# Kernel tuning notes

Measured on AMD Instinct MI355X. Metric: run time of the kernel, lower is better.

## Reference

```python
import jax, jax.numpy as jnp
import numpy as np

IO_DIM = 64
WIDTH = 16
HID = 128
N = 500000
BS = IO_DIM * WIDTH  # block size for u and w
OUT = 2 * BS + WIDTH  # hypernet output size


def setup_inputs() -> dict:
    key = jax.random.key(0)
    ks = jax.random.split(key, 8)
    s = 0.1  # small init so tanh stays in its active range
    return {
        "t": jax.random.uniform(ks[0], (1,), jnp.float32),
        "z": jax.random.normal(ks[1], (N, IO_DIM), jnp.float32),
        "W1": jax.random.normal(ks[2], (HID, 1), jnp.float32) * s,
        "b1": jnp.zeros((HID,), jnp.float32),
        "W2": jax.random.normal(ks[3], (HID, HID), jnp.float32) * s,
        "b2": jnp.zeros((HID,), jnp.float32),
        "W3": jax.random.normal(ks[4], (OUT, HID), jnp.float32) * s,
        "b3": jax.random.normal(ks[5], (OUT,), jnp.float32) * s,
    }


def reference(t, z, W1, b1, W2, b2, W3, b3):
    # Hypernetwork: scalar t -> (u, w, b) for each of WIDTH blocks.
    h = jnp.tanh(W1 @ t + b1)            # [HID]
    h = jnp.tanh(W2 @ h + b2)            # [HID]
    uwb = W3 @ h + b3                    # [2*BS + WIDTH]

    u = uwb[:BS].reshape(WIDTH, IO_DIM)        # u_k row vectors
    w = uwb[BS:2 * BS].reshape(WIDTH, IO_DIM)  # w_k column vectors
    bb = uwb[2 * BS:]                          # [WIDTH] biases

    # dz/dt = mean_k tanh(z . w_k + b_k) u_k
    a = z @ w.T + bb                     # [N, WIDTH]
    th = jnp.tanh(a)                     # [N, WIDTH]
    dz_dt = (th @ u) / WIDTH             # [N, IO_DIM]

    # Closed-form Jacobian trace (what the per-dim autograd loop computes):
    # tr(df/dz)_n = (1/WIDTH) sum_k sech^2(a_nk) * (u_k . w_k)
    uw = jnp.sum(u * w, axis=1)          # [WIDTH]
    trace = ((1.0 - th * th) @ uw) / WIDTH  # [N]
    dlogpz_dt = -trace[:, None]          # [N, 1]
    return dz_dt, dlogpz_dt
```

## Files before the change

### kernel.cpp

```cpp
#include <hip/hip_runtime.h>

#define IO_DIM 64
#define WIDTH 16
#define HID 128
#define BS_ 1024
#define NTH 256


typedef __attribute__((ext_vector_type(4))) float f32x4;
typedef __attribute__((ext_vector_type(8))) short bf16x8;

union U4 { unsigned u[4]; bf16x8 v; };

__device__ __forceinline__ unsigned cvt_pk_bf16(float lo, float hi) {
    unsigned r;
    asm("v_cvt_pk_bf16_f32 %0, %1, %2" : "=v"(r) : "v"(lo), "v"(hi));
    return r;
}

__device__ __forceinline__ float fast_tanh(float x) {
    float e = __expf(2.0f * x);
    return 1.0f - __fdividef(2.0f, e + 1.0f);
}

__device__ __forceinline__ void split8(const float* x, bf16x8& hi, bf16x8& lo) {
    U4 H, L;
    #pragma unroll
    for (int i = 0; i < 4; ++i) {
        unsigned h = cvt_pk_bf16(x[2 * i], x[2 * i + 1]);
        float h0 = __uint_as_float(h << 16);
        float h1 = __uint_as_float(h & 0xffff0000u);
        H.u[i] = h;
        L.u[i] = cvt_pk_bf16(x[2 * i] - h0, x[2 * i + 1] - h1);
    }
    hi = H.v; lo = L.v;
}

__global__ __launch_bounds__(128) void cnf_prep(
    const float* __restrict__ t, const float* __restrict__ W1,
    const float* __restrict__ b1, const float* __restrict__ W2,
    const float* __restrict__ b2, const float* __restrict__ W3,
    const float* __restrict__ b3, float* __restrict__ ws)
{
    __shared__ float h1[HID];
    __shared__ float h2[HID];
    __shared__ float su[64], sw[64];
    const int tid = threadIdx.x;

    h1[tid] = tanhf(W1[tid] * t[0] + b1[tid]);
    __syncthreads();

    {
        float s = b2[tid];
        const float4* W2v = (const float4*)(W2 + tid * HID);
        #pragma unroll 8
        for (int k = 0; k < HID / 4; ++k) {
            float4 wv = W2v[k];
            s = fmaf(wv.x, h1[4 * k + 0], s);
            s = fmaf(wv.y, h1[4 * k + 1], s);
            s = fmaf(wv.z, h1[4 * k + 2], s);
            s = fmaf(wv.w, h1[4 * k + 3], s);
        }
        h2[tid] = tanhf(s);
    }
    __syncthreads();

    const int b = blockIdx.x;
    if (b < 16) {
        const int half = tid >> 6;
        const int i = tid & 63;
        const int row = half * BS_ + b * 64 + i;
        float s = b3[row];
        const float4* W3v = (const float4*)(W3 + row * HID);
        #pragma unroll 8
        for (int k = 0; k < HID / 4; ++k) {
            float4 wv = W3v[k];
            s = fmaf(wv.x, h2[4 * k + 0], s);
            s = fmaf(wv.y, h2[4 * k + 1], s);
            s = fmaf(wv.z, h2[4 * k + 2], s);
            s = fmaf(wv.w, h2[4 * k + 3], s);
        }
        if (half == 0) {
            ws[1024 + i * 16 + b] = s * (1.0f / WIDTH);
            su[i] = s;
        } else {
            ws[i * 16 + b] = s;
            sw[i] = s;
        }
        __syncthreads();
        if (tid < 64) {
            float p = su[tid] * sw[tid];
            #pragma unroll
            for (int m = 32; m >= 1; m >>= 1) p += __shfl_xor(p, m, 64);
            if (tid == 0) ws[2064 + b] = -p * (1.0f / WIDTH);
        }
    } else {
        if (tid < WIDTH) {
            const int row = 2 * BS_ + tid;
            float s = b3[row];
            const float4* W3v = (const float4*)(W3 + row * HID);
            #pragma unroll 8
            for (int k = 0; k < HID / 4; ++k) {
                float4 wv = W3v[k];
                s = fmaf(wv.x, h2[4 * k + 0], s);
                s = fmaf(wv.y, h2[4 * k + 1], s);
                s = fmaf(wv.z, h2[4 * k + 2], s);
                s = fmaf(wv.w, h2[4 * k + 3], s);
            }
            ws[2048 + tid] = s;
        }
    }
}

__global__ __launch_bounds__(NTH) void cnf_main(
    const float* __restrict__ z, const float* __restrict__ ws,
    float* __restrict__ dz, float* __restrict__ dlog, int n)
{
    const int tid = threadIdx.x;
    const int wv  = tid >> 6;
    const int l   = tid & 63;
    const int q   = l >> 4;
    const int r15 = l & 15;
    const int wbase = blockIdx.x * NTH + wv * 64;

    bf16x8 whi[2], wlo[2];
    #pragma unroll
    for (int h = 0; h < 2; ++h) {
        float w8[8];
        #pragma unroll
        for (int e = 0; e < 8; ++e)
            w8[e] = ws[(h * 32 + q * 8 + e) * 16 + r15];
        split8(w8, whi[h], wlo[h]);
    }
    bf16x8 uhi[4], ulo[4];
    #pragma unroll
    for (int dt = 0; dt < 4; ++dt) {
        float u8[8];
        #pragma unroll
        for (int e = 0; e < 8; ++e)
            u8[e] = (q < 2) ? ws[1024 + (dt * 16 + r15) * 16 + q * 8 + e] : 0.0f;
        split8(u8, uhi[dt], ulo[dt]);
    }
    f32x4 bbv; float nuwv[4];
    #pragma unroll
    for (int rr = 0; rr < 4; ++rr) {
        bbv[rr]  = ws[2048 + q * 4 + rr];
        nuwv[rr] = ws[2064 + q * 4 + rr];
    }

    const float4* zg = (const float4*)z;

    float4 zA[2][4], zB[2][4];
    #pragma unroll
    for (int h = 0; h < 2; ++h) {
        #pragma unroll
        for (int g = 0; g < 4; ++g) {
            const int grow = min(wbase + g * 16 + r15, n - 1);
            const float4* p = zg + (size_t)grow * 16 + h * 8 + q * 2;
            zA[h][g] = p[0];
            zB[h][g] = p[1];
        }
    }

    f32x4 acc[4];
    #pragma unroll
    for (int g = 0; g < 4; ++g) acc[g] = bbv;

    #pragma unroll
    for (int h = 0; h < 2; ++h) {
        #pragma unroll
        for (int g = 0; g < 4; ++g) {
            const float4 a4 = zA[h][g], b4 = zB[h][g];
            float z8[8] = {a4.x, a4.y, a4.z, a4.w, b4.x, b4.y, b4.z, b4.w};
            bf16x8 zhi, zlo; split8(z8, zhi, zlo);
            acc[g] = __builtin_amdgcn_mfma_f32_16x16x32_bf16(whi[h], zhi, acc[g], 0, 0, 0);
            acc[g] = __builtin_amdgcn_mfma_f32_16x16x32_bf16(wlo[h], zhi, acc[g], 0, 0, 0);
            acc[g] = __builtin_amdgcn_mfma_f32_16x16x32_bf16(whi[h], zlo, acc[g], 0, 0, 0);
        }
    }

    float trs[4];
    const int sbase = ((2 * q) & 3) * 16 + r15;
    float4* dzv = (float4*)dz;

    #pragma unroll
    for (int g = 0; g < 4; ++g) {
        const float t0 = fast_tanh(acc[g][0]);
        const float t1 = fast_tanh(acc[g][1]);
        const float t2 = fast_tanh(acc[g][2]);
        const float t3 = fast_tanh(acc[g][3]);

        float tr = (1.0f - t0 * t0) * nuwv[0];
        tr = fmaf(1.0f - t1 * t1, nuwv[1], tr);
        tr = fmaf(1.0f - t2 * t2, nuwv[2], tr);
        tr = fmaf(1.0f - t3 * t3, nuwv[3], tr);
        tr += __shfl_xor(tr, 16);
        tr += __shfl_xor(tr, 32);
        trs[g] = tr;

        const int pk01 = (int)cvt_pk_bf16(t0, t1);
        const int pk23 = (int)cvt_pk_bf16(t2, t3);
        const int w0 = __shfl(pk01, sbase);
        const int w1 = __shfl(pk23, sbase);
        const int w2 = __shfl(pk01, sbase + 16);
        const int w3 = __shfl(pk23, sbase + 16);
        const bool act = (q < 2);
        U4 B;
        B.u[0] = act ? (unsigned)w0 : 0u;
        B.u[1] = act ? (unsigned)w1 : 0u;
        B.u[2] = act ? (unsigned)w2 : 0u;
        B.u[3] = act ? (unsigned)w3 : 0u;
        const bf16x8 b2 = B.v;

        f32x4 o[4];
        #pragma unroll
        for (int dt = 0; dt < 4; ++dt) {
            f32x4 zz = {0.f, 0.f, 0.f, 0.f};
            zz    = __builtin_amdgcn_mfma_f32_16x16x32_bf16(ulo[dt], b2, zz, 0, 0, 0);
            o[dt] = __builtin_amdgcn_mfma_f32_16x16x32_bf16(uhi[dt], b2, zz, 0, 0, 0);
        }
        const int grow = wbase + g * 16 + r15;
        if (grow < n) {
            #pragma unroll
            for (int dt = 0; dt < 4; ++dt) {
                float4 s = make_float4(o[dt][0], o[dt][1], o[dt][2], o[dt][3]);
                dzv[(size_t)grow * 16 + dt * 4 + q] = s;
            }
        }
    }

    float trf = trs[0];
    trf = (q == 1) ? trs[1] : trf;
    trf = (q == 2) ? trs[2] : trf;
    trf = (q == 3) ? trs[3] : trf;
    if (wbase + l < n) dlog[wbase + l] = trf;
}

extern "C" void kernel_launch(void* const* d_in, const int* in_sizes, int n_in,
                              void* d_out, int out_size, void* d_ws, size_t ws_size,
                              hipStream_t stream) {
    const float* t  = (const float*)d_in[0];
    const float* z  = (const float*)d_in[1];
    const float* W1 = (const float*)d_in[2];
    const float* b1 = (const float*)d_in[3];
    const float* W2 = (const float*)d_in[4];
    const float* b2 = (const float*)d_in[5];
    const float* W3 = (const float*)d_in[6];
    const float* b3 = (const float*)d_in[7];

    const int n = in_sizes[1] / IO_DIM;
    float* ws   = (float*)d_ws;
    float* out  = (float*)d_out;
    float* dzp  = out;
    float* dlog = out + (size_t)n * IO_DIM;

    cnf_prep<<<17, 128, 0, stream>>>(t, W1, b1, W2, b2, W3, b3, ws);

    const int grid = (n + NTH - 1) / NTH;
    cnf_main<<<grid, NTH, 0, stream>>>(z, ws, dzp, dlog, n);
}
```

Baseline: 61.13 us.

## Make main kernel persistent with grid-stride tiles and prefetch next z tile

```diff
diff --git a/kernel.cpp b/kernel.cpp
--- a/kernel.cpp
+++ b/kernel.cpp
@@ -5,6 +5,7 @@
 #define HID 128
 #define BS_ 1024
 #define NTH 256
+#define GRID_PERSIST 512
 
 
 typedef __attribute__((ext_vector_type(4))) float f32x4;
@@ -112,7 +113,7 @@
     }
 }
 
-__global__ __launch_bounds__(NTH) void cnf_main(
+__global__ __launch_bounds__(NTH, 2) void cnf_main(
     const float* __restrict__ z, const float* __restrict__ ws,
     float* __restrict__ dz, float* __restrict__ dlog, int n)
 {
@@ -121,7 +122,6 @@
     const int l   = tid & 63;
     const int q   = l >> 4;
     const int r15 = l & 15;
-    const int wbase = blockIdx.x * NTH + wv * 64;
 
     bf16x8 whi[2], wlo[2];
     #pragma unroll
@@ -148,92 +148,121 @@
         nuwv[rr] = ws[2064 + q * 4 + rr];
     }
 
+    const int ntiles = (n + 63) >> 6;
+    const int nw = gridDim.x * (NTH / 64);
+    int tile = blockIdx.x * (NTH / 64) + wv;
+    if (tile >= ntiles) return;
+
     const float4* zg = (const float4*)z;
+    float4* dzv = (float4*)dz;
+    const int sbase = ((2 * q) & 3) * 16 + r15;
 
     float4 zA[2][4], zB[2][4];
-    #pragma unroll
-    for (int h = 0; h < 2; ++h) {
+    {
+        const int wbase = tile * 64;
+        #pragma unroll
+        for (int h = 0; h < 2; ++h) {
+            #pragma unroll
+            for (int g = 0; g < 4; ++g) {
+                const int grow = min(wbase + g * 16 + r15, n - 1);
+                const float4* p = zg + (size_t)grow * 16 + h * 8 + q * 2;
+                zA[h][g] = p[0];
+                zB[h][g] = p[1];
+            }
+        }
+    }
+
+    for (;;) {
+        const int wbase = tile * 64;
+        const int nt = tile + nw;
+
+        f32x4 acc[4];
+        #pragma unroll
+        for (int g = 0; g < 4; ++g) acc[g] = bbv;
+
+        #pragma unroll
+        for (int h = 0; h < 2; ++h) {
+            #pragma unroll
+            for (int g = 0; g < 4; ++g) {
+                const float4 a4 = zA[h][g], b4 = zB[h][g];
+                float z8[8] = {a4.x, a4.y, a4.z, a4.w, b4.x, b4.y, b4.z, b4.w};
+                bf16x8 zhi, zlo; split8(z8, zhi, zlo);
+                acc[g] = __builtin_amdgcn_mfma_f32_16x16x32_bf16(whi[h], zhi, acc[g], 0, 0, 0);
+                acc[g] = __builtin_amdgcn_mfma_f32_16x16x32_bf16(wlo[h], zhi, acc[g], 0, 0, 0);
+                acc[g] = __builtin_amdgcn_mfma_f32_16x16x32_bf16(whi[h], zlo, acc[g], 0, 0, 0);
+            }
+        }
+
+        if (nt < ntiles) {
+            const int nb = nt * 64;
+            #pragma unroll
+            for (int h = 0; h < 2; ++h) {
+                #pragma unroll
+                for (int g = 0; g < 4; ++g) {
+                    const int grow = min(nb + g * 16 + r15, n - 1);
+                    const float4* p = zg + (size_t)grow * 16 + h * 8 + q * 2;
+                    zA[h][g] = p[0];
+                    zB[h][g] = p[1];
+                }
+            }
+        }
+
+        float trs[4];
         #pragma unroll
         for (int g = 0; g < 4; ++g) {
-            const int grow = min(wbase + g * 16 + r15, n - 1);
-            const float4* p = zg + (size_t)grow * 16 + h * 8 + q * 2;
-            zA[h][g] = p[0];
-            zB[h][g] = p[1];
-        }
-    }
-
-    f32x4 acc[4];
-    #pragma unroll
-    for (int g = 0; g < 4; ++g) acc[g] = bbv;
-
-    #pragma unroll
-    for (int h = 0; h < 2; ++h) {
-        #pragma unroll
-        for (int g = 0; g < 4; ++g) {
-            const float4 a4 = zA[h][g], b4 = zB[h][g];
-            float z8[8] = {a4.x, a4.y, a4.z, a4.w, b4.x, b4.y, b4.z, b4.w};
-            bf16x8 zhi, zlo; split8(z8, zhi, zlo);
-            acc[g] = __builtin_amdgcn_mfma_f32_16x16x32_bf16(whi[h], zhi, acc[g], 0, 0, 0);
-            acc[g] = __builtin_amdgcn_mfma_f32_16x16x32_bf16(wlo[h], zhi, acc[g], 0, 0, 0);
-            acc[g] = __builtin_amdgcn_mfma_f32_16x16x32_bf16(whi[h], zlo, acc[g], 0, 0, 0);
-        }
-    }
-
-    float trs[4];
-    const int sbase = ((2 * q) & 3) * 16 + r15;
-    float4* dzv = (float4*)dz;
-
-    #pragma unroll
-    for (int g = 0; g < 4; ++g) {
-        const float t0 = fast_tanh(acc[g][0]);
-        const float t1 = fast_tanh(acc[g][1]);
-        const float t2 = fast_tanh(acc[g][2]);
-        const float t3 = fast_tanh(acc[g][3]);
-
-        float tr = (1.0f - t0 * t0) * nuwv[0];
-        tr = fmaf(1.0f - t1 * t1, nuwv[1], tr);
-        tr = fmaf(1.0f - t2 * t2, nuwv[2], tr);
-        tr = fmaf(1.0f - t3 * t3, nuwv[3], tr);
-        tr += __shfl_xor(tr, 16);
-        tr += __shfl_xor(tr, 32);
-        trs[g] = tr;
-
-        const int pk01 = (int)cvt_pk_bf16(t0, t1);
-        const int pk23 = (int)cvt_pk_bf16(t2, t3);
-        const int w0 = __shfl(pk01, sbase);
-        const int w1 = __shfl(pk23, sbase);
-        const int w2 = __shfl(pk01, sbase + 16);
-        const int w3 = __shfl(pk23, sbase + 16);
-        const bool act = (q < 2);
-        U4 B;
-        B.u[0] = act ? (unsigned)w0 : 0u;
-        B.u[1] = act ? (unsigned)w1 : 0u;
-        B.u[2] = act ? (unsigned)w2 : 0u;
-        B.u[3] = act ? (unsigned)w3 : 0u;
-        const bf16x8 b2 = B.v;
-
-        f32x4 o[4];
-        #pragma unroll
-        for (int dt = 0; dt < 4; ++dt) {
-            f32x4 zz = {0.f, 0.f, 0.f, 0.f};
-            zz    = __builtin_amdgcn_mfma_f32_16x16x32_bf16(ulo[dt], b2, zz, 0, 0, 0);
-            o[dt] = __builtin_amdgcn_mfma_f32_16x16x32_bf16(uhi[dt], b2, zz, 0, 0, 0);
-        }
-        const int grow = wbase + g * 16 + r15;
-        if (grow < n) {
+            const float t0 = fast_tanh(acc[g][0]);
+            const float t1 = fast_tanh(acc[g][1]);
+            const float t2 = fast_tanh(acc[g][2]);
+            const float t3 = fast_tanh(acc[g][3]);
+
+            float tr = (1.0f - t0 * t0) * nuwv[0];
+            tr = fmaf(1.0f - t1 * t1, nuwv[1], tr);
+            tr = fmaf(1.0f - t2 * t2, nuwv[2], tr);
+            tr = fmaf(1.0f - t3 * t3, nuwv[3], tr);
+            tr += __shfl_xor(tr, 16);
+            tr += __shfl_xor(tr, 32);
+            trs[g] = tr;
+
+            const int pk01 = (int)cvt_pk_bf16(t0, t1);
+            const int pk23 = (int)cvt_pk_bf16(t2, t3);
+            const int w0 = __shfl(pk01, sbase);
+            const int w1 = __shfl(pk23, sbase);
+            const int w2 = __shfl(pk01, sbase + 16);
+            const int w3 = __shfl(pk23, sbase + 16);
+            const bool act = (q < 2);
+            U4 B;
+            B.u[0] = act ? (unsigned)w0 : 0u;
+            B.u[1] = act ? (unsigned)w1 : 0u;
+            B.u[2] = act ? (unsigned)w2 : 0u;
+            B.u[3] = act ? (unsigned)w3 : 0u;
+            const bf16x8 b2 = B.v;
+
+            f32x4 o[4];
             #pragma unroll
             for (int dt = 0; dt < 4; ++dt) {
-                float4 s = make_float4(o[dt][0], o[dt][1], o[dt][2], o[dt][3]);
-                dzv[(size_t)grow * 16 + dt * 4 + q] = s;
-            }
-        }
-    }
-
-    float trf = trs[0];
-    trf = (q == 1) ? trs[1] : trf;
-    trf = (q == 2) ? trs[2] : trf;
-    trf = (q == 3) ? trs[3] : trf;
-    if (wbase + l < n) dlog[wbase + l] = trf;
+                f32x4 zz = {0.f, 0.f, 0.f, 0.f};
+                zz    = __builtin_amdgcn_mfma_f32_16x16x32_bf16(ulo[dt], b2, zz, 0, 0, 0);
+                o[dt] = __builtin_amdgcn_mfma_f32_16x16x32_bf16(uhi[dt], b2, zz, 0, 0, 0);
+            }
+            const int grow = wbase + g * 16 + r15;
+            if (grow < n) {
+                #pragma unroll
+                for (int dt = 0; dt < 4; ++dt) {
+                    float4 s = make_float4(o[dt][0], o[dt][1], o[dt][2], o[dt][3]);
+                    dzv[(size_t)grow * 16 + dt * 4 + q] = s;
+                }
+            }
+        }
+
+        float trf = trs[0];
+        trf = (q == 1) ? trs[1] : trf;
+        trf = (q == 2) ? trs[2] : trf;
+        trf = (q == 3) ? trs[3] : trf;
+        if (wbase + l < n) dlog[wbase + l] = trf;
+
+        if (nt >= ntiles) break;
+        tile = nt;
+    }
 }
 
 extern "C" void kernel_launch(void* const* d_in, const int* in_sizes, int n_in,
@@ -256,6 +285,9 @@
 
     cnf_prep<<<17, 128, 0, stream>>>(t, W1, b1, W2, b2, W3, b3, ws);
 
-    const int grid = (n + NTH - 1) / NTH;
+    const int ntiles = (n + 63) >> 6;
+    int grid = GRID_PERSIST;
+    const int max_blocks = (ntiles + (NTH / 64) - 1) / (NTH / 64);
+    if (grid > max_blocks) grid = max_blocks;
     cnf_main<<<grid, NTH, 0, stream>>>(z, ws, dzp, dlog, n);
 }
```

Result: faster. 57.04 us (-6.7%).

## Make main kernel persistent with double-buffered z tile prefetch per wave

Applied to the files above, without the earlier changes.

```diff
diff --git a/kernel.cpp b/kernel.cpp
--- a/kernel.cpp
+++ b/kernel.cpp
@@ -5,6 +5,7 @@
 #define HID 128
 #define BS_ 1024
 #define NTH 256
+#define GRID_PERSIST 512
 
 
 typedef __attribute__((ext_vector_type(4))) float f32x4;
@@ -112,45 +113,11 @@
     }
 }
 
-__global__ __launch_bounds__(NTH) void cnf_main(
-    const float* __restrict__ z, const float* __restrict__ ws,
-    float* __restrict__ dz, float* __restrict__ dlog, int n)
-{
-    const int tid = threadIdx.x;
-    const int wv  = tid >> 6;
-    const int l   = tid & 63;
-    const int q   = l >> 4;
-    const int r15 = l & 15;
-    const int wbase = blockIdx.x * NTH + wv * 64;
-
-    bf16x8 whi[2], wlo[2];
-    #pragma unroll
-    for (int h = 0; h < 2; ++h) {
-        float w8[8];
-        #pragma unroll
-        for (int e = 0; e < 8; ++e)
-            w8[e] = ws[(h * 32 + q * 8 + e) * 16 + r15];
-        split8(w8, whi[h], wlo[h]);
-    }
-    bf16x8 uhi[4], ulo[4];
-    #pragma unroll
-    for (int dt = 0; dt < 4; ++dt) {
-        float u8[8];
-        #pragma unroll
-        for (int e = 0; e < 8; ++e)
-            u8[e] = (q < 2) ? ws[1024 + (dt * 16 + r15) * 16 + q * 8 + e] : 0.0f;
-        split8(u8, uhi[dt], ulo[dt]);
-    }
-    f32x4 bbv; float nuwv[4];
-    #pragma unroll
-    for (int rr = 0; rr < 4; ++rr) {
-        bbv[rr]  = ws[2048 + q * 4 + rr];
-        nuwv[rr] = ws[2064 + q * 4 + rr];
-    }
-
-    const float4* zg = (const float4*)z;
-
-    float4 zA[2][4], zB[2][4];
+
+__device__ __forceinline__ void load_tile(const float4* __restrict__ zg,
+                                          int wbase, int n, int r15, int q,
+                                          float4 (&zA)[2][4], float4 (&zB)[2][4])
+{
     #pragma unroll
     for (int h = 0; h < 2; ++h) {
         #pragma unroll
@@ -161,11 +128,15 @@
             zB[h][g] = p[1];
         }
     }
-
-    f32x4 acc[4];
+}
+
+__device__ __forceinline__ void phase1(const float4 (&zA)[2][4],
+                                       const float4 (&zB)[2][4],
+                                       const bf16x8 (&whi)[2], const bf16x8 (&wlo)[2],
+                                       const f32x4 bbv, f32x4 (&acc)[4])
+{
     #pragma unroll
     for (int g = 0; g < 4; ++g) acc[g] = bbv;
-
     #pragma unroll
     for (int h = 0; h < 2; ++h) {
         #pragma unroll
@@ -178,11 +149,16 @@
             acc[g] = __builtin_amdgcn_mfma_f32_16x16x32_bf16(whi[h], zlo, acc[g], 0, 0, 0);
         }
     }
-
+}
+
+__device__ __forceinline__ void phase2_store(const f32x4 (&acc)[4],
+                                             const bf16x8 (&uhi)[4], const bf16x8 (&ulo)[4],
+                                             const float (&nuwv)[4],
+                                             int wbase, int n, int l, int q, int r15,
+                                             int sbase, f32x4* __restrict__ dzv,
+                                             float* __restrict__ dlog)
+{
     float trs[4];
-    const int sbase = ((2 * q) & 3) * 16 + r15;
-    float4* dzv = (float4*)dz;
-
     #pragma unroll
     for (int g = 0; g < 4; ++g) {
         const float t0 = fast_tanh(acc[g][0]);
@@ -222,18 +198,82 @@
         const int grow = wbase + g * 16 + r15;
         if (grow < n) {
             #pragma unroll
-            for (int dt = 0; dt < 4; ++dt) {
-                float4 s = make_float4(o[dt][0], o[dt][1], o[dt][2], o[dt][3]);
-                dzv[(size_t)grow * 16 + dt * 4 + q] = s;
-            }
-        }
-    }
-
+            for (int dt = 0; dt < 4; ++dt)
+                dzv[(size_t)grow * 16 + dt * 4 + q] = o[dt];
+        }
+    }
     float trf = trs[0];
     trf = (q == 1) ? trs[1] : trf;
     trf = (q == 2) ? trs[2] : trf;
     trf = (q == 3) ? trs[3] : trf;
     if (wbase + l < n) dlog[wbase + l] = trf;
+}
+
+__global__ __launch_bounds__(NTH, 3) void cnf_main(
+    const float* __restrict__ z, const float* __restrict__ ws,
+    float* __restrict__ dz, float* __restrict__ dlog, int n)
+{
+    const int tid = threadIdx.x;
+    const int wv  = tid >> 6;
+    const int l   = tid & 63;
+    const int q   = l >> 4;
+    const int r15 = l & 15;
+
+    bf16x8 whi[2], wlo[2];
+    #pragma unroll
+    for (int h = 0; h < 2; ++h) {
+        float w8[8];
+        #pragma unroll
+        for (int e = 0; e < 8; ++e)
+            w8[e] = ws[(h * 32 + q * 8 + e) * 16 + r15];
+        split8(w8, whi[h], wlo[h]);
+    }
+    bf16x8 uhi[4], ulo[4];
+    #pragma unroll
+    for (int dt = 0; dt < 4; ++dt) {
+        float u8[8];
+        #pragma unroll
+        for (int e = 0; e < 8; ++e)
+            u8[e] = (q < 2) ? ws[1024 + (dt * 16 + r15) * 16 + q * 8 + e] : 0.0f;
+        split8(u8, uhi[dt], ulo[dt]);
+    }
+    f32x4 bbv; float nuwv[4];
+    #pragma unroll
+    for (int rr = 0; rr < 4; ++rr) {
+        bbv[rr]  = ws[2048 + q * 4 + rr];
+        nuwv[rr] = ws[2064 + q * 4 + rr];
+    }
+
+    const int ntiles = (n + 63) >> 6;
+    const int nw = gridDim.x * (NTH / 64);
+    int t0 = blockIdx.x * (NTH / 64) + wv;
+    if (t0 >= ntiles) return;
+    int t1 = t0 + nw;
+
+    const float4* zg = (const float4*)z;
+    f32x4* dzv = (f32x4*)dz;
+    const int sbase = ((2 * q) & 3) * 16 + r15;
+
+    float4 zA0[2][4], zB0[2][4], zA1[2][4], zB1[2][4];
+    load_tile(zg, t0 * 64, n, r15, q, zA0, zB0);
+    load_tile(zg, t1 * 64, n, r15, q, zA1, zB1);
+
+    f32x4 acc[4];
+    for (;;) {
+        phase1(zA0, zB0, whi, wlo, bbv, acc);
+        load_tile(zg, (t0 + 2 * nw) * 64, n, r15, q, zA0, zB0);
+        phase2_store(acc, uhi, ulo, nuwv, t0 * 64, n, l, q, r15, sbase, dzv, dlog);
+
+        if (t1 >= ntiles) break;
+
+        phase1(zA1, zB1, whi, wlo, bbv, acc);
+        load_tile(zg, (t1 + 2 * nw) * 64, n, r15, q, zA1, zB1);
+        phase2_store(acc, uhi, ulo, nuwv, t1 * 64, n, l, q, r15, sbase, dzv, dlog);
+
+        t0 += 2 * nw;
+        if (t0 >= ntiles) break;
+        t1 += 2 * nw;
+    }
 }
 
 extern "C" void kernel_launch(void* const* d_in, const int* in_sizes, int n_in,
@@ -256,6 +296,9 @@
 
     cnf_prep<<<17, 128, 0, stream>>>(t, W1, b1, W2, b2, W3, b3, ws);
 
-    const int grid = (n + NTH - 1) / NTH;
+    const int ntiles = (n + 63) >> 6;
+    int grid = GRID_PERSIST;
+    const int max_blocks = (ntiles + (NTH / 64) - 1) / (NTH / 64);
+    if (grid > max_blocks) grid = max_blocks;
     cnf_main<<<grid, NTH, 0, stream>>>(z, ws, dzp, dlog, n);
 }
```

New measurement: 112.9 us. +84.8%, slower.
